# Performance work log

Measured on AMD Instinct MI355X. Metric: run time of the kernel, lower is better.

## Reference

```python
import jax, jax.numpy as jnp
import numpy as np

LOG_STD_MIN, LOG_STD_MAX = -20.0, 2.0

B, OBS, ACT, M, HID = 131072, 17, 6, 8, 256


def setup_inputs() -> dict:
    key = jax.random.key(0)
    ks = jax.random.split(key, 10)
    w = lambda k, *sh: (jax.random.normal(k, sh, dtype=jnp.float32) * 0.05)
    z = lambda *sh: jnp.zeros(sh, dtype=jnp.float32)
    return {
        "obs": jax.random.normal(ks[0], (B, OBS), dtype=jnp.float32),
        # encoder MLP (two tanh layers; encoder.out is unused by forward)
        "enc_W1": w(ks[1], OBS, HID), "enc_b1": z(HID),
        "enc_W2": w(ks[2], HID, HID), "enc_b2": z(HID),
        # m per-chart Gaussian heads
        "head_muW": w(ks[3], M, HID, ACT), "head_mub": z(M, ACT),
        "head_logstd": z(M, ACT),
        # value head MLP
        "val_W1": w(ks[4], HID, HID), "val_b1": z(HID),
        "val_W2": w(ks[5], HID, HID), "val_b2": z(HID),
        "val_W3": w(ks[6], HID, 1), "val_b3": z(1),
        # chart cover (pre-initialized; non-trainable in torch module)
        "centers": jax.random.normal(ks[7], (M, HID), dtype=jnp.float32),
        "stats_mean": z(HID),
        "stats_var": jnp.ones((HID,), dtype=jnp.float32),
    }


def reference(obs, enc_W1, enc_b1, enc_W2, enc_b2,
              head_muW, head_mub, head_logstd,
              val_W1, val_b1, val_W2, val_b2, val_W3, val_b3,
              centers, stats_mean, stats_var):
    # shared encoder phi(o): two tanh layers -> feat [B, HID]
    h = jnp.tanh(obs @ enc_W1 + enc_b1)
    feat = jnp.tanh(h @ enc_W2 + enc_b2)

    # hard Voronoi chart routing on detached, whitened features
    zf = jax.lax.stop_gradient(feat)
    zw = (zf - stats_mean) * jax.lax.rsqrt(stats_var + 1e-6)
    # squared distances to centers: [B, M] (argmin of d^2 == argmin of d)
    d2 = (jnp.sum(zw * zw, axis=-1, keepdims=True)
          - 2.0 * (zw @ centers.T)
          + jnp.sum(centers * centers, axis=-1))
    hard_idx = jnp.argmin(d2, axis=1)  # [B]

    # per-chart Gaussian heads, then gather the selected head per sample
    mu_all = jnp.einsum('bd,mda->bma', feat, head_muW) + head_mub  # [B, M, ACT]
    mu = jnp.take_along_axis(mu_all, hard_idx[:, None, None], axis=1)[:, 0, :]
    log_std = jnp.clip(head_logstd[hard_idx], LOG_STD_MIN, LOG_STD_MAX)  # [B, ACT]

    # value head V(feat)
    v1 = jnp.tanh(feat @ val_W1 + val_b1)
    v2 = jnp.tanh(v1 @ val_W2 + val_b2)
    v = (v2 @ val_W3 + val_b3)[:, 0]  # [B]

    # policy params (post-clamp, as stored in SquashedDiagGaussian) + value
    return jnp.concatenate([mu, log_std, v[:, None]], axis=-1)  # [B, 2*ACT+1]
```

## Files before the change

### kernel.cpp

```cpp
#include <hip/hip_runtime.h>
#include <math.h>

typedef __attribute__((ext_vector_type(8))) short bf16x8;
typedef __attribute__((ext_vector_type(4))) float f32x4;

#define B_TOT 131072
#define NOBS 17
#define NACT 6
#define NM 8
#define HID 256
#define TS 64
#define NT 512
#define NW 8
#define NOUT 13
#define EPS_MARGIN 0.20f
#define CAPF 65536

#define AST 264
#define OST 40
#define MUST 52
#define SCST 12

#define OFF_FLAGS 64
#define OFF_W1H  (OFF_FLAGS + 4*CAPF)
#define OFF_W1L  (OFF_W1H + 256*32*2)
#define OFF_W2T  (OFF_W1L + 256*32*2)
#define OFF_V1T  (OFF_W2T + 256*256*2)
#define OFF_V2T  (OFF_V1T + 256*256*2)
#define OFF_HDT  (OFF_V2T + 256*256*2)
#define OFF_G0   (OFF_HDT + 64*256*2)
#define WS_NEED  (OFF_G0 + 64)

__device__ __forceinline__ unsigned short f2bf(float f) {
  unsigned int u = __float_as_uint(f);
  u = (u + 0x7fffu + ((u >> 16) & 1u)) >> 16;
  return (unsigned short)u;
}
__device__ __forceinline__ float bf2f(unsigned short h) {
  return __uint_as_float(((unsigned int)h) << 16);
}
__device__ __forceinline__ float tanh_fast2(float x) {
  float e = __expf(2.0f * x);
  float r = __builtin_amdgcn_rcpf(e + 1.0f);
  return 1.0f - 2.0f * r;
}
__device__ __forceinline__ unsigned int pk2(float a, float b) {
  unsigned int r;
  asm("v_cvt_pk_bf16_f32 %0, %1, %2" : "=v"(r) : "v"(a), "v"(b));
  return r;
}
__device__ __forceinline__ f32x4 MFMA(bf16x8 a, bf16x8 b, f32x4 c) {
  return __builtin_amdgcn_mfma_f32_16x16x32_bf16(a, b, c, 0, 0, 0);
}

extern "C" __global__ void ppo_zero(int* cnt) {
  if (cnt && threadIdx.x == 0) cnt[0] = 0;
}

extern "C" __global__ __launch_bounds__(256)
void ppo_prep(const float* __restrict__ eW1, const float* __restrict__ eW2,
              const float* __restrict__ vW1, const float* __restrict__ vW2,
              const float* __restrict__ muW, const float* __restrict__ cen,
              const float* __restrict__ smean, const float* __restrict__ svar,
              unsigned char* wsb, int* cnt)
{
  if (blockIdx.x == 864) {
    int m = threadIdx.x >> 5, l = threadIdx.x & 31;
    double acc = 0.0;
    for (int k = l; k < HID; k += 32) {
      double s = 1.0 / sqrt((double)svar[k] + 1e-6);
      double c = (double)cen[m * HID + k];
      acc += c * (2.0 * (double)smean[k] * s + c);
    }
#pragma unroll
    for (int w = 16; w >= 1; w >>= 1) acc += __shfl_xor(acc, w, 32);
    if (l == 0) ((float*)(wsb + OFF_G0))[m] = (float)acc;
    if (threadIdx.x == 0) cnt[0] = 0;
    return;
  }
  int t = blockIdx.x * 256 + threadIdx.x;
  if (t < 65536) {
    int c = t >> 8, k = t & 255;
    ((unsigned short*)(wsb + OFF_W2T))[c * 256 + k] = f2bf(eW2[k * 256 + c]);
  } else if (t < 131072) {
    int u = t - 65536; int c = u >> 8, k = u & 255;
    ((unsigned short*)(wsb + OFF_V1T))[c * 256 + k] = f2bf(vW1[k * 256 + c]);
  } else if (t < 196608) {
    int u = t - 131072; int c = u >> 8, k = u & 255;
    ((unsigned short*)(wsb + OFF_V2T))[c * 256 + k] = f2bf(vW2[k * 256 + c]);
  } else if (t < 212992) {
    int u = t - 196608; int c = u >> 8, k = u & 255;
    float v = 0.f;
    if (c < 48) { int m = c / 6, a = c - 6 * m; v = muW[(m * 256 + k) * 6 + a]; }
    else if (c < 56) {
      int m = c - 48;
      double s = 1.0 / sqrt((double)svar[k] + 1e-6);
      v = (float)(-2.0 * s * (double)cen[m * 256 + k]);
    }
    ((unsigned short*)(wsb + OFF_HDT))[c * 256 + k] = f2bf(v);
  } else if (t < 221184) {
    int u = t - 212992; int c = u >> 5, k = u & 31;
    float v = (k < NOBS) ? eW1[k * 256 + c] : 0.f;
    unsigned short hi = f2bf(v);
    ((unsigned short*)(wsb + OFF_W1H))[c * 32 + k] = hi;
    ((unsigned short*)(wsb + OFF_W1L))[c * 32 + k] = f2bf(v - bf2f(hi));
  }
}

template<int CT>
__device__ __forceinline__ void gemm256(const unsigned short* __restrict__ WT,
                                        const unsigned short* act,
                                        int cb, int l15, int h, f32x4 acc[CT][4])
{
#pragma unroll
  for (int kt = 0; kt < 8; ++kt) {
    int kk = kt * 32 + 8 * h;
    bf16x8 a[CT], b[4];
#pragma unroll
    for (int ct = 0; ct < CT; ++ct)
      a[ct] = *(const bf16x8*)(WT + (cb + 16 * ct + l15) * 256 + kk);
#pragma unroll
    for (int nt = 0; nt < 4; ++nt)
      b[nt] = *(const bf16x8*)(act + (16 * nt + l15) * AST + kk);
#pragma unroll
    for (int ct = 0; ct < CT; ++ct)
#pragma unroll
      for (int nt = 0; nt < 4; ++nt)
        acc[ct][nt] = MFMA(a[ct], b[nt], acc[ct][nt]);
  }
}

__device__ __forceinline__ void epi_tanh_store(f32x4 acc[2][4], unsigned short* dst,
                                               int cb, int l15, int h)
{
#pragma unroll
  for (int ct = 0; ct < 2; ++ct)
#pragma unroll
    for (int nt = 0; nt < 4; ++nt) {
      float t0 = tanh_fast2(acc[ct][nt][0]);
      float t1 = tanh_fast2(acc[ct][nt][1]);
      float t2 = tanh_fast2(acc[ct][nt][2]);
      float t3 = tanh_fast2(acc[ct][nt][3]);
      uint2 u; u.x = pk2(t0, t1); u.y = pk2(t2, t3);
      *(uint2*)(dst + (16 * nt + l15) * AST + cb + 16 * ct + 4 * h) = u;
    }
}

extern "C" __global__ __launch_bounds__(NT, 4)
void ppo_mfma(const float* __restrict__ obs,
              const float* __restrict__ eb1, const float* __restrict__ eb2,
              const float* __restrict__ mub, const float* __restrict__ logstd,
              const float* __restrict__ vb1, const float* __restrict__ vb2,
              const float* __restrict__ vW3, const float* __restrict__ vb3,
              const unsigned char* __restrict__ wsb,
              float* __restrict__ out, int* cnt, int* flags, int cap)
{
  __shared__ unsigned short Hb[TS * AST];
  __shared__ unsigned short Fb[TS * AST];
  __shared__ unsigned short MU[TS * MUST];
  __shared__ float SC[TS * SCST];
  __shared__ float VP[NW * TS];
  __shared__ float LS[48];

  const int tid = threadIdx.x, lane = tid & 63, wid = tid >> 6;
  const int l15 = lane & 15, h = lane >> 4;
  const int cb = wid * 32;
  const int s0 = blockIdx.x * TS;

  const unsigned short* W1H = (const unsigned short*)(wsb + OFF_W1H);
  const unsigned short* W1L = (const unsigned short*)(wsb + OFF_W1L);
  const unsigned short* W2T = (const unsigned short*)(wsb + OFF_W2T);
  const unsigned short* V1T = (const unsigned short*)(wsb + OFF_V1T);
  const unsigned short* V2T = (const unsigned short*)(wsb + OFF_V2T);
  const unsigned short* HDT = (const unsigned short*)(wsb + OFF_HDT);
  const float* g0g = (const float*)(wsb + OFF_G0);

  unsigned short* OBH = Fb;
  unsigned short* OBL = Fb + TS * OST;

  bf16x8 aH[2], aL[2];
#pragma unroll
  for (int ct = 0; ct < 2; ++ct) {
    aH[ct] = *(const bf16x8*)(W1H + (cb + 16 * ct + l15) * 32 + 8 * h);
    aL[ct] = *(const bf16x8*)(W1L + (cb + 16 * ct + l15) * 32 + 8 * h);
  }

  for (int t = tid; t < TS * NOBS; t += NT) {
    int s = t / NOBS, k = t - NOBS * s;
    float v = obs[(size_t)s0 * NOBS + t];
    unsigned short hi = f2bf(v);
    OBH[s * OST + k] = hi;
    OBL[s * OST + k] = f2bf(v - bf2f(hi));
  }
  for (int t = tid; t < TS * (32 - NOBS); t += NT) {
    int s = t / (32 - NOBS), k = NOBS + t - (32 - NOBS) * s;
    OBH[s * OST + k] = 0; OBL[s * OST + k] = 0;
  }
  if (tid < 48) LS[tid] = fminf(fmaxf(logstd[tid], -20.f), 2.f);
  __syncthreads();

  {
    f32x4 acc[2][4];
    f32x4 b0 = *(const f32x4*)(eb1 + cb + 4 * h);
    f32x4 b1 = *(const f32x4*)(eb1 + cb + 16 + 4 * h);
#pragma unroll
    for (int nt = 0; nt < 4; ++nt) { acc[0][nt] = b0; acc[1][nt] = b1; }
    bf16x8 bH[4], bL[4];
#pragma unroll
    for (int nt = 0; nt < 4; ++nt) {
      bH[nt] = *(const bf16x8*)(OBH + (16 * nt + l15) * OST + 8 * h);
      bL[nt] = *(const bf16x8*)(OBL + (16 * nt + l15) * OST + 8 * h);
    }
#pragma unroll
    for (int ct = 0; ct < 2; ++ct)
#pragma unroll
      for (int nt = 0; nt < 4; ++nt) {
        acc[ct][nt] = MFMA(aH[ct], bH[nt], acc[ct][nt]);
        acc[ct][nt] = MFMA(aL[ct], bH[nt], acc[ct][nt]);
        acc[ct][nt] = MFMA(aH[ct], bL[nt], acc[ct][nt]);
      }
    epi_tanh_store(acc, Hb, cb, l15, h);
  }
  __syncthreads();

  {
    f32x4 acc[2][4];
    f32x4 b0 = *(const f32x4*)(eb2 + cb + 4 * h);
    f32x4 b1 = *(const f32x4*)(eb2 + cb + 16 + 4 * h);
#pragma unroll
    for (int nt = 0; nt < 4; ++nt) { acc[0][nt] = b0; acc[1][nt] = b1; }
    gemm256<2>(W2T, Hb, cb, l15, h, acc);
    epi_tanh_store(acc, Fb, cb, l15, h);
  }
  __syncthreads();

  if (wid < 4) {
    f32x4 hacc[1][4];
    f32x4 hb;
    if (wid < 3)      hb = *(const f32x4*)(mub + 16 * wid + 4 * h);
    else if (h < 2)   hb = *(const f32x4*)(g0g + 4 * h);
    else              hb = (f32x4){0.f, 0.f, 0.f, 0.f};
#pragma unroll
    for (int nt = 0; nt < 4; ++nt) hacc[0][nt] = hb;
    gemm256<1>(HDT, Fb, 16 * wid, l15, h, hacc);
    if (wid < 3) {
#pragma unroll
      for (int nt = 0; nt < 4; ++nt) {
        uint2 u;
        u.x = pk2(hacc[0][nt][0], hacc[0][nt][1]);
        u.y = pk2(hacc[0][nt][2], hacc[0][nt][3]);
        *(uint2*)(MU + (16 * nt + l15) * MUST + 16 * wid + 4 * h) = u;
      }
    } else if (h < 2) {
#pragma unroll
      for (int nt = 0; nt < 4; ++nt)
        *(f32x4*)(SC + (16 * nt + l15) * SCST + 4 * h) = hacc[0][nt];
    }
  }
  {
    f32x4 acc[2][4];
    f32x4 b0 = *(const f32x4*)(vb1 + cb + 4 * h);
    f32x4 b1 = *(const f32x4*)(vb1 + cb + 16 + 4 * h);
#pragma unroll
    for (int nt = 0; nt < 4; ++nt) { acc[0][nt] = b0; acc[1][nt] = b1; }
    gemm256<2>(V1T, Fb, cb, l15, h, acc);
    epi_tanh_store(acc, Hb, cb, l15, h);
  }
  __syncthreads();

  {
    f32x4 acc[2][4];
    f32x4 b0 = *(const f32x4*)(vb2 + cb + 4 * h);
    f32x4 b1 = *(const f32x4*)(vb2 + cb + 16 + 4 * h);
#pragma unroll
    for (int nt = 0; nt < 4; ++nt) { acc[0][nt] = b0; acc[1][nt] = b1; }
    gemm256<2>(V2T, Hb, cb, l15, h, acc);
    f32x4 w30 = *(const f32x4*)(vW3 + cb + 4 * h);
    f32x4 w31 = *(const f32x4*)(vW3 + cb + 16 + 4 * h);
#pragma unroll
    for (int nt = 0; nt < 4; ++nt) {
      float v = 0.f;
#pragma unroll
      for (int r = 0; r < 4; ++r) {
        v = fmaf(tanh_fast2(acc[0][nt][r]), w30[r], v);
        v = fmaf(tanh_fast2(acc[1][nt][r]), w31[r], v);
      }
      v += __shfl_xor(v, 16);
      v += __shfl_xor(v, 32);
      if (h == 0) VP[wid * TS + 16 * nt + l15] = v;
    }
  }
  __syncthreads();

  if (wid == 0) {
    int s = lane;
    int best = 0;
    float bs = SC[s * SCST], bs2 = 3.4e38f;
#pragma unroll
    for (int m = 1; m < NM; ++m) {
      float sm = SC[s * SCST + m];
      if (sm < bs) { bs2 = bs; bs = sm; best = m; }
      else if (sm < bs2) bs2 = sm;
    }
    if (cnt && (bs2 - bs) < EPS_MARGIN) {
      int idx = atomicAdd(cnt, 1);
      if (idx < cap) flags[idx] = s0 + s;
    }
    float v = vb3[0];
#pragma unroll
    for (int w = 0; w < NW; ++w) v += VP[w * TS + s];
    float* orow = out + (size_t)(s0 + s) * NOUT;
#pragma unroll
    for (int a = 0; a < NACT; ++a) orow[a] = bf2f(MU[s * MUST + best * NACT + a]);
#pragma unroll
    for (int a = 0; a < NACT; ++a) orow[NACT + a] = LS[best * NACT + a];
    orow[2 * NACT] = v;
  }
}

extern "C" __global__ __launch_bounds__(256, 2)
void ppo_recheck(const float* __restrict__ obs,
                 const float* __restrict__ eW1, const float* __restrict__ eb1,
                 const float* __restrict__ eW2, const float* __restrict__ eb2,
                 const float* __restrict__ muW, const float* __restrict__ mub,
                 const float* __restrict__ logstd,
                 const float* __restrict__ cen, const float* __restrict__ smean,
                 const float* __restrict__ svar,
                 float* __restrict__ out,
                 const int* cnt, const int* flags, int cap)
{
  if (!cnt) return;
  __shared__ double hbuf[HID];
  __shared__ double fbuf[HID];
  __shared__ double d2buf[NM];
  __shared__ double obsd[NOBS];
  __shared__ int bestv;
  const int tid = threadIdx.x;
  const int n = min(cnt[0], cap);

  for (int i = blockIdx.x; i < n; i += gridDim.x) {
    const int s = flags[i];
    if (tid < NOBS) obsd[tid] = (double)obs[(size_t)s * NOBS + tid];
    __syncthreads();
    double a1 = (double)eb1[tid];
    for (int k = 0; k < NOBS; ++k) a1 = fma(obsd[k], (double)eW1[k * HID + tid], a1);
    hbuf[tid] = tanh(a1);
    __syncthreads();
    double a2 = (double)eb2[tid];
    for (int k = 0; k < HID; ++k) a2 = fma(hbuf[k], (double)eW2[k * HID + tid], a2);
    fbuf[tid] = tanh(a2);
    __syncthreads();
    {
      int g = tid >> 5, l = tid & 31;
      double dot = 0.0, zn = 0.0, cn = 0.0;
      for (int j = 0; j < HID / 32; ++j) {
        int k = l + j * 32;
        double zs = 1.0 / sqrt((double)svar[k] + 1e-6);
        double zw = (fbuf[k] - (double)smean[k]) * zs;
        double ck = (double)cen[g * HID + k];
        dot = fma(zw, ck, dot);
        zn  = fma(zw, zw, zn);
        cn  = fma(ck, ck, cn);
      }
      for (int m = 16; m >= 1; m >>= 1) {
        dot += __shfl_xor(dot, m, 32);
        zn  += __shfl_xor(zn,  m, 32);
        cn  += __shfl_xor(cn,  m, 32);
      }
      if (l == 0) d2buf[g] = zn - 2.0 * dot + cn;
    }
    __syncthreads();
    if (tid == 0) {
      int best = 0;
      double bs = d2buf[0];
      for (int m = 1; m < NM; ++m)
        if (d2buf[m] < bs) { bs = d2buf[m]; best = m; }
      bestv = best;
    }
    __syncthreads();
    const int best = bestv;
    if (tid < NACT) {
      float acc = mub[best * NACT + tid];
      for (int k = 0; k < HID; ++k)
        acc = fmaf((float)fbuf[k], muW[(best * HID + k) * NACT + tid], acc);
      out[(size_t)s * NOUT + tid] = acc;
    } else if (tid < 2 * NACT) {
      int a = tid - NACT;
      float ls = logstd[best * NACT + a];
      out[(size_t)s * NOUT + NACT + a] = fminf(fmaxf(ls, -20.0f), 2.0f);
    }
    __syncthreads();
  }
}

extern "C" __global__ __launch_bounds__(NT, 4)
void ppo_fp32_fb(const float* __restrict__ obs,
                 const float* __restrict__ eW1, const float* __restrict__ eb1,
                 const float* __restrict__ eW2, const float* __restrict__ eb2,
                 const float* __restrict__ muW, const float* __restrict__ mub,
                 const float* __restrict__ logstd,
                 const float* __restrict__ vW1, const float* __restrict__ vb1,
                 const float* __restrict__ vW2, const float* __restrict__ vb2,
                 const float* __restrict__ vW3, const float* __restrict__ vb3,
                 const float* __restrict__ cen, const float* __restrict__ smean,
                 const float* __restrict__ svar,
                 float* __restrict__ out, int* cnt, int* flags, int cap)
{
  __shared__ float act[HID * TS];
  __shared__ float mubuf[NM * TS * NACT];
  __shared__ float scbuf[NM * TS];
  __shared__ float zsbuf[HID];
  const int tid  = threadIdx.x;
  const int lane = tid & 63;
  const int wid  = tid >> 6;
  const int c0   = wid * 32;
  const int s0   = blockIdx.x * TS;
  float* obs_s = mubuf;
  for (int idx = tid; idx < TS * NOBS; idx += NT) {
    int s = idx / NOBS, i = idx - s * NOBS;
    obs_s[i * TS + s] = obs[s0 * NOBS + idx];
  }
  if (tid < HID) zsbuf[tid] = (float)(1.0 / sqrt((double)svar[tid] + 1e-6));
  __syncthreads();
  {
    float acc[32];
#pragma unroll
    for (int c = 0; c < 32; ++c) acc[c] = eb1[c0 + c];
    float ob[NOBS];
#pragma unroll
    for (int i = 0; i < NOBS; ++i) ob[i] = obs_s[i * TS + lane];
#pragma unroll
    for (int i = 0; i < NOBS; ++i) {
      const float* w = &eW1[i * HID + c0];
#pragma unroll
      for (int c = 0; c < 32; ++c) acc[c] = fmaf(ob[i], w[c], acc[c]);
    }
#pragma unroll
    for (int c = 0; c < 32; ++c) act[(c0 + c) * TS + lane] = tanh_fast2(acc[c]);
  }
  __syncthreads();
  {
    float acc[32];
#pragma unroll
    for (int c = 0; c < 32; ++c) acc[c] = eb2[c0 + c];
#pragma unroll 4
    for (int k = 0; k < HID; ++k) {
      float a = act[k * TS + lane];
      const float* w = &eW2[k * HID + c0];
#pragma unroll
      for (int c = 0; c < 32; ++c) acc[c] = fmaf(a, w[c], acc[c]);
    }
    __syncthreads();
#pragma unroll
    for (int c = 0; c < 32; ++c) act[(c0 + c) * TS + lane] = tanh_fast2(acc[c]);
  }
  __syncthreads();
  {
    double dot = 0.0, zn = 0.0, cn = 0.0;
    float mu[NACT];
#pragma unroll
    for (int a = 0; a < NACT; ++a) mu[a] = mub[wid * NACT + a];
#pragma unroll 2
    for (int k = 0; k < HID; ++k) {
      float f = act[k * TS + lane];
      double zw = ((double)f - (double)smean[k]) * (double)zsbuf[k];
      double ck = (double)cen[wid * HID + k];
      dot = fma(zw, ck, dot); zn = fma(zw, zw, zn); cn = fma(ck, ck, cn);
      const float* w = &muW[(wid * HID + k) * NACT];
#pragma unroll
      for (int a = 0; a < NACT; ++a) mu[a] = fmaf(f, w[a], mu[a]);
    }
    scbuf[wid * TS + lane] = (float)(zn - 2.0 * dot + cn);
#pragma unroll
    for (int a = 0; a < NACT; ++a) mubuf[(wid * TS + lane) * NACT + a] = mu[a];
  }
  {
    float acc[32];
#pragma unroll
    for (int c = 0; c < 32; ++c) acc[c] = vb1[c0 + c];
#pragma unroll 4
    for (int k = 0; k < HID; ++k) {
      float f = act[k * TS + lane];
      const float* w = &vW1[k * HID + c0];
#pragma unroll
      for (int c = 0; c < 32; ++c) acc[c] = fmaf(f, w[c], acc[c]);
    }
    __syncthreads();
#pragma unroll
    for (int c = 0; c < 32; ++c) act[(c0 + c) * TS + lane] = tanh_fast2(acc[c]);
  }
  __syncthreads();
  {
    float acc[32];
#pragma unroll
    for (int c = 0; c < 32; ++c) acc[c] = vb2[c0 + c];
#pragma unroll 4
    for (int k = 0; k < HID; ++k) {
      float f = act[k * TS + lane];
      const float* w = &vW2[k * HID + c0];
#pragma unroll
      for (int c = 0; c < 32; ++c) acc[c] = fmaf(f, w[c], acc[c]);
    }
    __syncthreads();
#pragma unroll
    for (int c = 0; c < 32; ++c) act[(c0 + c) * TS + lane] = tanh_fast2(acc[c]);
  }
  __syncthreads();
  if (wid == 0) {
    int best = 0;
    float bs = scbuf[lane], bs2 = 3.4e38f;
#pragma unroll
    for (int m = 1; m < NM; ++m) {
      float sm = scbuf[m * TS + lane];
      if (sm < bs) { bs2 = bs; bs = sm; best = m; }
      else if (sm < bs2) bs2 = sm;
    }
    if (cnt && (bs2 - bs) < 1e-2f) {
      int idx = atomicAdd(cnt, 1);
      if (idx < cap) flags[idx] = s0 + lane;
    }
    float v = vb3[0];
#pragma unroll 4
    for (int k = 0; k < HID; ++k) v = fmaf(act[k * TS + lane], vW3[k], v);
    float* orow = &out[(size_t)(s0 + lane) * NOUT];
#pragma unroll
    for (int a = 0; a < NACT; ++a) orow[a] = mubuf[(best * TS + lane) * NACT + a];
#pragma unroll
    for (int a = 0; a < NACT; ++a) {
      float ls = logstd[best * NACT + a];
      orow[NACT + a] = fminf(fmaxf(ls, -20.0f), 2.0f);
    }
    orow[2 * NACT] = v;
  }
}

extern "C" void kernel_launch(void* const* d_in, const int* in_sizes, int n_in,
                              void* d_out, int out_size, void* d_ws, size_t ws_size,
                              hipStream_t stream) {
  const float* obs   = (const float*)d_in[0];
  const float* eW1   = (const float*)d_in[1];
  const float* eb1   = (const float*)d_in[2];
  const float* eW2   = (const float*)d_in[3];
  const float* eb2   = (const float*)d_in[4];
  const float* muW   = (const float*)d_in[5];
  const float* mub   = (const float*)d_in[6];
  const float* lstd  = (const float*)d_in[7];
  const float* vW1   = (const float*)d_in[8];
  const float* vb1   = (const float*)d_in[9];
  const float* vW2   = (const float*)d_in[10];
  const float* vb2   = (const float*)d_in[11];
  const float* vW3   = (const float*)d_in[12];
  const float* vb3   = (const float*)d_in[13];
  const float* cen   = (const float*)d_in[14];
  const float* smean = (const float*)d_in[15];
  const float* svar  = (const float*)d_in[16];
  float* out = (float*)d_out;
  unsigned char* wsb = (unsigned char*)d_ws;

  if (ws_size >= (size_t)WS_NEED) {
    int* cnt = (int*)wsb;
    int* flags = (int*)(wsb + OFF_FLAGS);
    hipLaunchKernelGGL(ppo_prep, dim3(865), dim3(256), 0, stream,
                       eW1, eW2, vW1, vW2, muW, cen, smean, svar, wsb, cnt);
    hipLaunchKernelGGL(ppo_mfma, dim3(B_TOT / TS), dim3(NT), 0, stream,
                       obs, eb1, eb2, mub, lstd, vb1, vb2, vW3, vb3,
                       (const unsigned char*)wsb, out, cnt, flags, CAPF);
    hipLaunchKernelGGL(ppo_recheck, dim3(2048), dim3(256), 0, stream,
                       obs, eW1, eb1, eW2, eb2, muW, mub, lstd,
                       cen, smean, svar, out, cnt, flags, CAPF);
  } else {
    int* cnt = nullptr; int* flags = nullptr; int cap = 0;
    if (ws_size >= 1024) {
      cnt = (int*)wsb;
      flags = cnt + 16;
      size_t c = (ws_size - 64) / 4;
      cap = (int)(c < (size_t)CAPF ? c : (size_t)CAPF);
    }
    hipLaunchKernelGGL(ppo_zero, dim3(1), dim3(64), 0, stream, cnt);
    hipLaunchKernelGGL(ppo_fp32_fb, dim3(B_TOT / TS), dim3(NT), 0, stream,
                       obs, eW1, eb1, eW2, eb2, muW, mub, lstd,
                       vW1, vb1, vW2, vb2, vW3, vb3, cen, smean, svar, out,
                       cnt, flags, cap);
    hipLaunchKernelGGL(ppo_recheck, dim3(2048), dim3(256), 0, stream,
                       obs, eW1, eb1, eW2, eb2, muW, mub, lstd,
                       cen, smean, svar, out, cnt, flags, cap);
  }
}
```

Before: 229.7 us.

## Fuse near-tie chart recheck into main MFMA kernel using per-block LDS flag list

Removes the separate recheck kernel launch and the global atomic flag list. Each block now collects near-tie samples into a shared-memory list, then recomputes those samples in fp64 inside the same kernel, reusing the Hb buffer as scratch. The W1 fragment loads are also moved inside the first GEMM scope to shorten register live ranges. The cost is a serial per-sample recheck loop with many block barriers in blocks that have ties, which can stall that block and increase tail latency.

```diff
diff --git a/kernel.cpp b/kernel.cpp
--- a/kernel.cpp
+++ b/kernel.cpp
@@ -153,14 +153,19 @@
               const float* __restrict__ vb1, const float* __restrict__ vb2,
               const float* __restrict__ vW3, const float* __restrict__ vb3,
               const unsigned char* __restrict__ wsb,
-              float* __restrict__ out, int* cnt, int* flags, int cap)
+              const float* __restrict__ eW1f, const float* __restrict__ eW2f,
+              const float* __restrict__ muWf, const float* __restrict__ cenf,
+              const float* __restrict__ smeanf, const float* __restrict__ svarf,
+              float* __restrict__ out)
 {
-  __shared__ unsigned short Hb[TS * AST];
+  __shared__ __attribute__((aligned(16))) unsigned short Hb[TS * AST];
   __shared__ unsigned short Fb[TS * AST];
   __shared__ unsigned short MU[TS * MUST];
   __shared__ float SC[TS * SCST];
   __shared__ float VP[NW * TS];
   __shared__ float LS[48];
+  __shared__ int FCNT;
+  __shared__ int FLS[64];
 
   const int tid = threadIdx.x, lane = tid & 63, wid = tid >> 6;
   const int l15 = lane & 15, h = lane >> 4;
@@ -178,13 +183,6 @@
   unsigned short* OBH = Fb;
   unsigned short* OBL = Fb + TS * OST;
 
-  bf16x8 aH[2], aL[2];
-#pragma unroll
-  for (int ct = 0; ct < 2; ++ct) {
-    aH[ct] = *(const bf16x8*)(W1H + (cb + 16 * ct + l15) * 32 + 8 * h);
-    aL[ct] = *(const bf16x8*)(W1L + (cb + 16 * ct + l15) * 32 + 8 * h);
-  }
-
   for (int t = tid; t < TS * NOBS; t += NT) {
     int s = t / NOBS, k = t - NOBS * s;
     float v = obs[(size_t)s0 * NOBS + t];
@@ -205,7 +203,12 @@
     f32x4 b1 = *(const f32x4*)(eb1 + cb + 16 + 4 * h);
 #pragma unroll
     for (int nt = 0; nt < 4; ++nt) { acc[0][nt] = b0; acc[1][nt] = b1; }
-    bf16x8 bH[4], bL[4];
+    bf16x8 aH[2], aL[2], bH[4], bL[4];
+#pragma unroll
+    for (int ct = 0; ct < 2; ++ct) {
+      aH[ct] = *(const bf16x8*)(W1H + (cb + 16 * ct + l15) * 32 + 8 * h);
+      aL[ct] = *(const bf16x8*)(W1L + (cb + 16 * ct + l15) * 32 + 8 * h);
+    }
 #pragma unroll
     for (int nt = 0; nt < 4; ++nt) {
       bH[nt] = *(const bf16x8*)(OBH + (16 * nt + l15) * OST + 8 * h);
@@ -268,6 +271,7 @@
   }
   __syncthreads();
 
+  if (tid == 0) FCNT = 0;
   {
     f32x4 acc[2][4];
     f32x4 b0 = *(const f32x4*)(vb2 + cb + 4 * h);
@@ -302,9 +306,9 @@
       if (sm < bs) { bs2 = bs; bs = sm; best = m; }
       else if (sm < bs2) bs2 = sm;
     }
-    if (cnt && (bs2 - bs) < EPS_MARGIN) {
-      int idx = atomicAdd(cnt, 1);
-      if (idx < cap) flags[idx] = s0 + s;
+    if ((bs2 - bs) < EPS_MARGIN) {
+      int idx = atomicAdd(&FCNT, 1);
+      FLS[idx] = s;
     }
     float v = vb3[0];
 #pragma unroll
@@ -315,6 +319,73 @@
 #pragma unroll
     for (int a = 0; a < NACT; ++a) orow[NACT + a] = LS[best * NACT + a];
     orow[2 * NACT] = v;
+  }
+  __syncthreads();
+
+  const int nf = FCNT;
+  if (nf == 0) return;
+  double* hbuf  = (double*)Hb;
+  double* fbuf  = hbuf + HID;
+  double* d2buf = fbuf + HID;
+  double* obsd  = d2buf + NM;
+  int*    bestp = (int*)(obsd + NOBS);
+
+  for (int i = 0; i < nf; ++i) {
+    const size_t s = (size_t)(s0 + FLS[i]);
+    if (tid < NOBS) obsd[tid] = (double)obs[s * NOBS + tid];
+    __syncthreads();
+    if (tid < HID) {
+      double a1 = (double)eb1[tid];
+      for (int k = 0; k < NOBS; ++k) a1 = fma(obsd[k], (double)eW1f[k * HID + tid], a1);
+      hbuf[tid] = tanh(a1);
+    }
+    __syncthreads();
+    if (tid < HID) {
+      double a2 = (double)eb2[tid];
+      for (int k = 0; k < HID; ++k) a2 = fma(hbuf[k], (double)eW2f[k * HID + tid], a2);
+      fbuf[tid] = tanh(a2);
+    }
+    __syncthreads();
+    if (tid < HID) {
+      int g = tid >> 5, l = tid & 31;
+      double dot = 0.0, zn = 0.0, cn = 0.0;
+      for (int j = 0; j < HID / 32; ++j) {
+        int k = l + j * 32;
+        double zs = 1.0 / sqrt((double)svarf[k] + 1e-6);
+        double zw = (fbuf[k] - (double)smeanf[k]) * zs;
+        double ck = (double)cenf[g * HID + k];
+        dot = fma(zw, ck, dot);
+        zn  = fma(zw, zw, zn);
+        cn  = fma(ck, ck, cn);
+      }
+      for (int m = 16; m >= 1; m >>= 1) {
+        dot += __shfl_xor(dot, m, 32);
+        zn  += __shfl_xor(zn,  m, 32);
+        cn  += __shfl_xor(cn,  m, 32);
+      }
+      if (l == 0) d2buf[g] = zn - 2.0 * dot + cn;
+    }
+    __syncthreads();
+    if (tid == 0) {
+      int b = 0;
+      double bsd = d2buf[0];
+      for (int m = 1; m < NM; ++m)
+        if (d2buf[m] < bsd) { bsd = d2buf[m]; b = m; }
+      bestp[0] = b;
+    }
+    __syncthreads();
+    const int b = bestp[0];
+    if (tid < NACT) {
+      float acc = mub[b * NACT + tid];
+      for (int k = 0; k < HID; ++k)
+        acc = fmaf((float)fbuf[k], muWf[(b * HID + k) * NACT + tid], acc);
+      out[s * NOUT + tid] = acc;
+    } else if (tid < 2 * NACT) {
+      int a = tid - NACT;
+      float ls = logstd[b * NACT + a];
+      out[s * NOUT + NACT + a] = fminf(fmaxf(ls, -20.0f), 2.0f);
+    }
+    __syncthreads();
   }
 }
 
@@ -559,15 +630,12 @@
 
   if (ws_size >= (size_t)WS_NEED) {
     int* cnt = (int*)wsb;
-    int* flags = (int*)(wsb + OFF_FLAGS);
     hipLaunchKernelGGL(ppo_prep, dim3(865), dim3(256), 0, stream,
                        eW1, eW2, vW1, vW2, muW, cen, smean, svar, wsb, cnt);
     hipLaunchKernelGGL(ppo_mfma, dim3(B_TOT / TS), dim3(NT), 0, stream,
                        obs, eb1, eb2, mub, lstd, vb1, vb2, vW3, vb3,
-                       (const unsigned char*)wsb, out, cnt, flags, CAPF);
-    hipLaunchKernelGGL(ppo_recheck, dim3(2048), dim3(256), 0, stream,
-                       obs, eW1, eb1, eW2, eb2, muW, mub, lstd,
-                       cen, smean, svar, out, cnt, flags, CAPF);
+                       (const unsigned char*)wsb,
+                       eW1, eW2, muW, cen, smean, svar, out);
   } else {
     int* cnt = nullptr; int* flags = nullptr; int cap = 0;
     if (ws_size >= 1024) {
```

Result: slower. 370.4 us (+61.3%).
